# Optimization experiments

Hardware: AMD Instinct MI355X
Metric: run time of the kernel (lower is better)

## Reference

```python
import jax, jax.numpy as jnp
import numpy as np

HEAD = 4
EPS = 1e-12


def _l2norm(x, axis):
    # torch F.normalize: x / max(||x||_2, eps)
    return x / jnp.maximum(jnp.linalg.norm(x, axis=axis, keepdims=True), EPS)


def setup_inputs() -> dict:
    key = jax.random.key(0)
    ks = jax.random.split(key, 12)
    n, t, c, h, w = 2, 7, 96, 96, 96
    inp = {
        "curr_feat": jax.random.normal(ks[0], (n, c, h, w), jnp.float32),
        "index_feat_set_s1": jax.random.normal(ks[1], (n, t, c, h, w), jnp.float32),
        "anchor_feat": jax.random.normal(ks[2], (n, c, h, w), jnp.float32),
        "sparse_feat_set_s1": jax.random.normal(ks[3], (n, t, c, h, w), jnp.float32),
        "sparse_feat_set_s2": jax.random.normal(ks[4], (n, t, c, h, w), jnp.float32),
        "sparse_feat_set_s3": jax.random.normal(ks[5], (n, t, c, h, w), jnp.float32),
        # absolute pixel coordinates (x,y interleaved per frame), mostly in-bounds
        # with a little overshoot to exercise zeros padding of grid_sample
        "location_feat": jax.random.uniform(ks[6], (n, t * 2, h, w), jnp.float32, minval=-2.0, maxval=float(w) + 1.0),
        "proj_w": 0.02 * jax.random.normal(ks[7], (c, c), jnp.float32),
        "proj_b": jnp.zeros((c,), jnp.float32),
        "fusion_w": 0.02 * jax.random.normal(ks[8], (c, 3 * c), jnp.float32),
        "fusion_b": jnp.zeros((c,), jnp.float32),
    }
    return inp


def reference(curr_feat, index_feat_set_s1, anchor_feat, sparse_feat_set_s1,
              sparse_feat_set_s2, sparse_feat_set_s3, location_feat,
              proj_w, proj_b, fusion_w, fusion_b):
    n, c, h, w = anchor_feat.shape
    t = sparse_feat_set_s1.shape[1]
    hd = c // HEAD
    hw = h * w

    # ---- flow-guided nearest grid_sample (align_corners=True, zeros pad) ----
    loc = location_feat.reshape(n, t, 2, h, w)  # (n,t,2,h,w): [x, y] pixel coords
    gx = 2.0 * loc[:, :, 0] / max(w - 1, 1) - 1.0
    gy = 2.0 * loc[:, :, 1] / max(h - 1, 1) - 1.0
    ix = jnp.round((gx + 1.0) * 0.5 * (w - 1))  # nearest (round-half-even, as torch)
    iy = jnp.round((gy + 1.0) * 0.5 * (h - 1))
    valid = (ix >= 0) & (ix <= w - 1) & (iy >= 0) & (iy <= h - 1)
    lin = (jnp.clip(iy, 0, h - 1).astype(jnp.int32) * w
           + jnp.clip(ix, 0, w - 1).astype(jnp.int32)).reshape(n, t, 1, hw)
    vmask = valid.reshape(n, t, 1, hw)

    def sample(f):  # f: (n,t,c,h,w) -> gathered (n,t,c,hw)
        g = jnp.take_along_axis(f.reshape(n, t, c, hw), lin, axis=3)
        return jnp.where(vmask, g, 0.0)

    samp1 = sample(sparse_feat_set_s1)
    samp2 = sample(sparse_feat_set_s2)
    samp3 = sample(sparse_feat_set_s3)
    sampi = sample(index_feat_set_s1)

    # ---- per-pixel multi-head max-correlation over t frames ----
    # queries: normalize over full channel dim c BEFORE splitting into heads
    q = _l2norm(curr_feat.reshape(n, c, hw).transpose(0, 2, 1), -1).reshape(n, hw, HEAD, hd)
    k = _l2norm(sampi.transpose(0, 3, 1, 2), -1).reshape(n, hw, t, HEAD, hd)
    scores = jnp.einsum('npthd,nphd->npht', k, q)  # scale == 1.0 in mode='max'
    corr_soft = jnp.max(scores, axis=3)     # (n,hw,head)
    corr_index = jnp.argmax(scores, axis=3)  # (n,hw,head), first-max like torch

    soft_img = jnp.broadcast_to(corr_soft[..., None], (n, hw, HEAD, hd)) \
                  .reshape(n, h, w, c).transpose(0, 3, 1, 2)  # (n,c,h,w)
    idx = jnp.broadcast_to(corr_index[..., None], (n, hw, HEAD, hd)) \
             .reshape(n, hw, c).transpose(0, 2, 1)[:, None]  # (n,1,c,hw)

    def pick(samp):  # select winning frame per (channel-group, pixel)
        return jnp.take_along_axis(samp, idx, axis=1)[:, 0].reshape(n, c, h, w)

    cat = jnp.concatenate([pick(samp1), pick(samp2), pick(samp3)], axis=1)  # (n,3c,h,w)
    out = jnp.einsum('ndhw,cd->nchw', cat, fusion_w) + fusion_b[None, :, None, None]
    out = out * soft_img
    out = jnp.einsum('nchw,dc->ndhw', out, proj_w) + proj_b[None, :, None, None]
    return out + anchor_feat
```

## Files before the change

### kernel.cpp

```cpp
#include <hip/hip_runtime.h>
#include <hip/hip_bf16.h>

#define N_    2
#define T_    7
#define C_    96
#define H_    96
#define W_    96
#define HW_   9216
#define HEAD_ 4
#define HD_   24
#define C3_   288
#define P_    16
#define QP_   100
#define CATP_ 292
#define NBLK_ (N_ * (HW_ / P_))
#define PLANES_ 14
#define CHUNK_  64
#define NCHUNK_ 144

typedef unsigned int u32;

__device__ __forceinline__ float bits2f(u32 b) {
    union { u32 u; float f; } x; x.u = b; return x.f;
}

__device__ __forceinline__ unsigned short f2bf(float f) {
    union { __hip_bfloat16 h; unsigned short s; } u;
    u.h = __float2bfloat16(f);
    return u.s;
}

template<bool BF16>
__device__ __forceinline__ float ld1(const void* p, int i) {
    if constexpr (BF16) return bits2f(((u32)((const unsigned short*)p)[i]) << 16);
    else                return ((const float*)p)[i];
}

template<bool BF16>
__device__ __forceinline__ void ld4w(const void* p, int i, float w[4]) {
    if constexpr (BF16) {
        const uint2 u = ((const uint2*)p)[i >> 2];
        w[0] = bits2f(u.x << 16);
        w[1] = bits2f(u.x & 0xFFFF0000u);
        w[2] = bits2f(u.y << 16);
        w[3] = bits2f(u.y & 0xFFFF0000u);
    } else {
        const float4 v = *((const float4*)((const float*)p + i));
        w[0] = v.x; w[1] = v.y; w[2] = v.z; w[3] = v.w;
    }
}

template<bool BF16>
__device__ __forceinline__ void st1(void* p, int i, float v) {
    if constexpr (BF16) ((unsigned short*)p)[i] = f2bf(v);
    else                ((float*)p)[i] = v;
}

template<bool BF16>
__device__ __forceinline__ void st4w(void* p, int i, const float v[4]) {
    if constexpr (BF16) {
        uint2 w;
        w.x = (u32)f2bf(v[0]) | ((u32)f2bf(v[1]) << 16);
        w.y = (u32)f2bf(v[2]) | ((u32)f2bf(v[3]) << 16);
        ((uint2*)p)[i >> 2] = w;
    } else {
        *((float4*)((float*)p + i)) = make_float4(v[0], v[1], v[2], v[3]);
    }
}

__device__ __forceinline__ bool block_detect_bf16(const u32* __restrict__ w,
                                                  int tid, int* s_flag) {
    if (tid < 64) {
        u32 x = w[tid];
        u32 f = x & 0x7FFFu;
        int inwin = (f >= 0x3A00u) && (f <= 0x4200u);
        unsigned long long m = __ballot(inwin);
        if (tid == 0) *s_flag = (__popcll(m) >= 40) ? 1 : 0;
    }
    __syncthreads();
    return *s_flag != 0;
}

template<bool BF16>
__device__ __forceinline__ void transp_body(const void* __restrict__ src,
                                            void* __restrict__ dst,
                                            int bx, int tid, char* tileraw) {
    const int pl = bx / NCHUNK_;
    const int x0 = (bx - pl * NCHUNK_) * CHUNK_;
    if constexpr (BF16) {
        unsigned short (*tile)[CHUNK_ + 2] = (unsigned short (*)[CHUNK_ + 2])tileraw;
        const unsigned short* s = (const unsigned short*)src;
        unsigned short* d = (unsigned short*)dst;
        for (int i = tid; i < C_ * (CHUNK_ / 4); i += 256) {
            int ch = i >> 4, xq = i & 15;
            const ushort4 v = *((const ushort4*)(s + (pl * C_ + ch) * HW_ + x0 + 4 * xq));
            tile[ch][4 * xq + 0] = v.x; tile[ch][4 * xq + 1] = v.y;
            tile[ch][4 * xq + 2] = v.z; tile[ch][4 * xq + 3] = v.w;
        }
        __syncthreads();
        for (int i = tid; i < CHUNK_ * (C_ / 4); i += 256) {
            int p = i / 24, cq = i - p * 24;
            ushort4 v;
            v.x = tile[4 * cq + 0][p]; v.y = tile[4 * cq + 1][p];
            v.z = tile[4 * cq + 2][p]; v.w = tile[4 * cq + 3][p];
            *((ushort4*)(d + (pl * HW_ + x0 + p) * C_ + 4 * cq)) = v;
        }
    } else {
        float (*tile)[CHUNK_ + 1] = (float (*)[CHUNK_ + 1])tileraw;
        const float* s = (const float*)src;
        float* d = (float*)dst;
        for (int i = tid; i < C_ * (CHUNK_ / 4); i += 256) {
            int ch = i >> 4, xq = i & 15;
            const float4 v = *((const float4*)(s + (pl * C_ + ch) * HW_ + x0 + 4 * xq));
            tile[ch][4 * xq + 0] = v.x; tile[ch][4 * xq + 1] = v.y;
            tile[ch][4 * xq + 2] = v.z; tile[ch][4 * xq + 3] = v.w;
        }
        __syncthreads();
        for (int i = tid; i < CHUNK_ * (C_ / 4); i += 256) {
            int p = i / 24, cq = i - p * 24;
            float4 v;
            v.x = tile[4 * cq + 0][p]; v.y = tile[4 * cq + 1][p];
            v.z = tile[4 * cq + 2][p]; v.w = tile[4 * cq + 3][p];
            *((float4*)(d + (pl * HW_ + x0 + p) * C_ + 4 * cq)) = v;
        }
    }
}

__global__ __launch_bounds__(256) void transp_kernel(
    const void* __restrict__ a0, const void* __restrict__ a1,
    const void* __restrict__ a2, const void* __restrict__ a3,
    void* __restrict__ dstb, unsigned long long szb,
    const u32* __restrict__ detect_src)
{
    __shared__ __align__(16) char tileraw[C_ * (CHUNK_ + 1) * 4];
    __shared__ int s_flag;
    const int arr = blockIdx.y;
    const void* src = (arr == 0) ? a0 : (arr == 1) ? a1 : (arr == 2) ? a2 : a3;
    void* dst = (char*)dstb + (unsigned long long)arr * szb;
    const int tid = threadIdx.x;
    const bool bf = block_detect_bf16(detect_src, tid, &s_flag);
    if (bf) transp_body<true >(src, dst, blockIdx.x, tid, tileraw);
    else    transp_body<false>(src, dst, blockIdx.x, tid, tileraw);
}

template<bool BF16, bool TGB>
__device__ __forceinline__ void argmax_body(
    const void* __restrict__ curr, const void* __restrict__ loc,
    const void* __restrict__ kT,
    float* __restrict__ ws_best, int* __restrict__ ws_gbase,
    float* s_u, int (*s_lin)[P_], float (*s_red)[8],
    float (*s_best)[HEAD_], int (*s_bidx)[HEAD_], float* s_inv)
{
#define S_Q(pp, ch)  s_u[(pp) * QP_ + (ch)]
#define S_K(pp, ch)  s_u[P_ * QP_ + (pp) * QP_ + (ch)]
    const int tid = threadIdx.x;
    const int b  = blockIdx.x;
    const int nn = b / (HW_ / P_);
    const int p0 = (b - nn * (HW_ / P_)) * P_;

    if (tid < T_ * P_) {
        int t = tid / P_, pp = tid - t * P_;
        int p = p0 + pp;
        float x = ld1<BF16>(loc, (nn * 2 * T_ + 2 * t    ) * HW_ + p);
        float y = ld1<BF16>(loc, (nn * 2 * T_ + 2 * t + 1) * HW_ + p);
        float gx = 2.0f * x / 95.0f - 1.0f;
        float gy = 2.0f * y / 95.0f - 1.0f;
        float fx = (gx + 1.0f) * 0.5f * 95.0f;
        float fy = (gy + 1.0f) * 0.5f * 95.0f;
        float ix = rintf(fx), iy = rintf(fy);
        bool v = (ix >= 0.0f) && (ix <= 95.0f) && (iy >= 0.0f) && (iy <= 95.0f);
        s_lin[t][pp] = v ? ((int)iy * W_ + (int)ix) : -1;
    }
    if (tid >= 128 && tid < 128 + P_ * HEAD_) {
        int q = tid - 128;
        s_best[q >> 2][q & 3] = -3.0e38f; s_bidx[q >> 2][q & 3] = 0;
    }

    for (int i = tid; i < C_ * (P_ / 4); i += 256) {
        int ch = i >> 2, pq = i & 3;
        float w[4];
        ld4w<BF16>(curr, (nn * C_ + ch) * HW_ + p0 + 4 * pq, w);
        S_Q(4 * pq + 0, ch) = w[0]; S_Q(4 * pq + 1, ch) = w[1];
        S_Q(4 * pq + 2, ch) = w[2]; S_Q(4 * pq + 3, ch) = w[3];
    }
    __syncthreads();

    if (tid < P_ * 8) {
        int pp = tid >> 3, j = tid & 7;
        float s = 0.f;
        #pragma unroll
        for (int k = 0; k < 12; ++k) { float v = S_Q(pp, j * 12 + k); s += v * v; }
        s_red[pp][j] = s;
    }
    __syncthreads();
    if (tid < P_) {
        float s = 0.f;
        #pragma unroll
        for (int j = 0; j < 8; ++j) s += s_red[tid][j];
        s_inv[tid] = 1.0f / fmaxf(sqrtf(s), 1e-12f);
    }
    __syncthreads();
    for (int i = tid; i < C_ * P_; i += 256) {
        int pp = i & (P_ - 1), ch = i >> 4;
        S_Q(pp, ch) *= s_inv[pp];
    }

    for (int t = 0; t < T_; ++t) {
        __syncthreads();
        for (int i = tid; i < 24 * P_; i += 256) {
            int pp = i / 24, j = i - pp * 24;
            int lin = s_lin[t][pp];
            float w[4] = {0.f, 0.f, 0.f, 0.f};
            if (lin >= 0) ld4w<BF16>(kT, ((nn * T_ + t) * HW_ + lin) * C_ + 4 * j, w);
            *((float4*)&S_K(pp, 4 * j)) = make_float4(w[0], w[1], w[2], w[3]);
        }
        __syncthreads();
        if (tid < P_ * 8) {
            int pp = tid >> 3, j = tid & 7;
            float s = 0.f;
            #pragma unroll
            for (int k = 0; k < 12; ++k) { float v = S_K(pp, j * 12 + k); s += v * v; }
            s_red[pp][j] = s;
        }
        __syncthreads();
        if (tid < P_) {
            float s = 0.f;
            #pragma unroll
            for (int j = 0; j < 8; ++j) s += s_red[tid][j];
            s_inv[tid] = 1.0f / fmaxf(sqrtf(s), 1e-12f);
        }
        __syncthreads();
        if (tid < P_ * HEAD_) {
            int pp = tid >> 2, h = tid & 3;
            float s = 0.f;
            #pragma unroll
            for (int dq = 0; dq < 6; ++dq) {
                const float4 kv = *((const float4*)&S_K(pp, h * HD_ + 4 * dq));
                const float4 qv = *((const float4*)&S_Q(pp, h * HD_ + 4 * dq));
                s += kv.x * qv.x; s += kv.y * qv.y; s += kv.z * qv.z; s += kv.w * qv.w;
            }
            s *= s_inv[pp];
            if (s > s_best[pp][h]) { s_best[pp][h] = s; s_bidx[pp][h] = t; }
        }
    }
    if (tid < P_ * HEAD_) {
        int pp = tid >> 2, h = tid & 3;
        int bt = s_bidx[pp][h];
        int lin = s_lin[bt][pp];
        int g = (nn * HW_ + p0 + pp) * HEAD_ + h;
        ws_best[g] = s_best[pp][h];
        int gb;
        if (lin < 0)       gb = -1;
        else if (TGB)      gb = ((nn * T_ + bt) * HW_ + lin) * C_;
        else               gb = (nn * T_ + bt) * C_ * HW_ + lin;
        ws_gbase[g] = gb;
    }
#undef S_Q
#undef S_K
}

template<bool TGB>
__global__ __launch_bounds__(256, 8) void argmax_kernel(
    const void* __restrict__ curr, const void* __restrict__ loc,
    const void* __restrict__ kT,
    float* __restrict__ ws_best, int* __restrict__ ws_gbase)
{
    __shared__ __align__(16) float s_u[2 * P_ * QP_];
    __shared__ int   s_lin[T_][P_];
    __shared__ float s_red[P_][8];
    __shared__ float s_best[P_][HEAD_];
    __shared__ int   s_bidx[P_][HEAD_];
    __shared__ float s_inv[P_];
    __shared__ int   s_flag;
    const bool bf = block_detect_bf16((const u32*)curr, threadIdx.x, &s_flag);
    if (bf) argmax_body<true , TGB>(curr, loc, kT, ws_best, ws_gbase, s_u, s_lin, s_red, s_best, s_bidx, s_inv);
    else    argmax_body<false, TGB>(curr, loc, kT, ws_best, ws_gbase, s_u, s_lin, s_red, s_best, s_bidx, s_inv);
}

template<bool BF16, bool TRANS>
__device__ __forceinline__ void catgemv_body(
    const void* __restrict__ anchor, const void* __restrict__ s1,
    const void* __restrict__ s2, const void* __restrict__ s3,
    const void* __restrict__ pw, const void* __restrict__ pb,
    const void* __restrict__ fw, const void* __restrict__ fb,
    void* __restrict__ outp,
    const float* __restrict__ ws_best, const int* __restrict__ ws_gbase,
    float* s_u, float (*s_mid)[QP_], float (*s_best)[HEAD_], int (*s_gbase)[HEAD_])
{
#define S_CAT(pp, d) s_u[(pp) * CATP_ + (d)]
    const int tid = threadIdx.x;
    const int b  = blockIdx.x;
    const int nn = b / (HW_ / P_);
    const int p0 = (b - nn * (HW_ / P_)) * P_;

    if (tid < P_ * HEAD_) {
        int pp = tid >> 2, h = tid & 3;
        int g = (nn * HW_ + p0 + pp) * HEAD_ + h;
        s_best[pp][h]  = ws_best[g];
        s_gbase[pp][h] = ws_gbase[g];
    }
    __syncthreads();

    if constexpr (TRANS) {
        for (int i = tid; i < P_ * 72; i += 256) {
            int px = i / 72, j = i - px * 72;
            int set = j / 24, jj = j - set * 24;
            int gb = s_gbase[px][jj / 6];
            float w[4] = {0.f, 0.f, 0.f, 0.f};
            if (gb >= 0) {
                const void* sp = (set == 0) ? s1 : (set == 1) ? s2 : s3;
                ld4w<BF16>(sp, gb + 4 * jj, w);
            }
            *((float4*)&S_CAT(px, set * C_ + 4 * jj)) = make_float4(w[0], w[1], w[2], w[3]);
        }
    } else {
        for (int i = tid; i < C3_ * P_; i += 256) {
            int pp = i / C3_, d = i - pp * C3_;
            int set = d / C_, ch = d - set * C_;
            int gb = s_gbase[pp][ch / HD_];
            float v = 0.f;
            if (gb >= 0) {
                const void* sp = (set == 0) ? s1 : (set == 1) ? s2 : s3;
                v = ld1<BF16>(sp, gb + ch * HW_);
            }
            S_CAT(pp, d) = v;
        }
    }
    __syncthreads();

    if (tid < 192) {
        const int cp = tid >> 2, pq = tid & 3;
        const int co0 = cp * 2, px0 = pq * 4;
        float acc[2][4];
        #pragma unroll
        for (int r = 0; r < 2; ++r)
            #pragma unroll
            for (int k = 0; k < 4; ++k) acc[r][k] = 0.f;
        for (int d = 0; d < C3_; d += 4) {
            float4 cv[4];
            #pragma unroll
            for (int k = 0; k < 4; ++k) cv[k] = *((const float4*)&S_CAT(px0 + k, d));
            #pragma unroll
            for (int r = 0; r < 2; ++r) {
                float w[4]; ld4w<BF16>(fw, (co0 + r) * C3_ + d, w);
                #pragma unroll
                for (int k = 0; k < 4; ++k)
                    acc[r][k] += w[0] * cv[k].x + w[1] * cv[k].y + w[2] * cv[k].z + w[3] * cv[k].w;
            }
        }
        const int hh = co0 / HD_;
        #pragma unroll
        for (int r = 0; r < 2; ++r) {
            float fbv = ld1<BF16>(fb, co0 + r);
            #pragma unroll
            for (int k = 0; k < 4; ++k)
                s_mid[px0 + k][co0 + r] = (acc[r][k] + fbv) * s_best[px0 + k][hh];
        }
    }
    __syncthreads();

    if (tid < 192) {
        const int dp = tid >> 2, pq = tid & 3;
        const int do0 = dp * 2, px0 = pq * 4;
        float acc[2][4];
        #pragma unroll
        for (int r = 0; r < 2; ++r)
            #pragma unroll
            for (int k = 0; k < 4; ++k) acc[r][k] = 0.f;
        for (int c = 0; c < C_; c += 4) {
            float4 mv[4];
            #pragma unroll
            for (int k = 0; k < 4; ++k) mv[k] = *((const float4*)&s_mid[px0 + k][c]);
            #pragma unroll
            for (int r = 0; r < 2; ++r) {
                float w[4]; ld4w<BF16>(pw, (do0 + r) * C_ + c, w);
                #pragma unroll
                for (int k = 0; k < 4; ++k)
                    acc[r][k] += w[0] * mv[k].x + w[1] * mv[k].y + w[2] * mv[k].z + w[3] * mv[k].w;
            }
        }
        #pragma unroll
        for (int r = 0; r < 2; ++r) {
            float pbv = ld1<BF16>(pb, do0 + r);
            float av[4];
            ld4w<BF16>(anchor, (nn * C_ + do0 + r) * HW_ + p0 + px0, av);
            float res[4];
            #pragma unroll
            for (int k = 0; k < 4; ++k) res[k] = acc[r][k] + pbv + av[k];
            st4w<BF16>(outp, (nn * C_ + do0 + r) * HW_ + p0 + px0, res);
        }
    }
#undef S_CAT
}

template<bool TRANS>
__global__ __launch_bounds__(256, 6) void catgemv_kernel(
    const void* __restrict__ curr, const void* __restrict__ anchor,
    const void* __restrict__ s1, const void* __restrict__ s2,
    const void* __restrict__ s3, const void* __restrict__ pw,
    const void* __restrict__ pb, const void* __restrict__ fw,
    const void* __restrict__ fb, void* __restrict__ outp,
    const float* __restrict__ ws_best, const int* __restrict__ ws_gbase)
{
    __shared__ __align__(16) float s_u[P_ * CATP_];
    __shared__ __align__(16) float s_mid[P_][QP_];
    __shared__ float s_best[P_][HEAD_];
    __shared__ int   s_gbase[P_][HEAD_];
    __shared__ int   s_flag;
    const bool bf = block_detect_bf16((const u32*)curr, threadIdx.x, &s_flag);
    if (bf) catgemv_body<true , TRANS>(anchor, s1, s2, s3, pw, pb, fw, fb, outp, ws_best, ws_gbase,
                                       s_u, s_mid, s_best, s_gbase);
    else    catgemv_body<false, TRANS>(anchor, s1, s2, s3, pw, pb, fw, fb, outp, ws_best, ws_gbase,
                                       s_u, s_mid, s_best, s_gbase);
}

template<bool BF16>
__device__ __forceinline__ void mono_body(
    const void* __restrict__ curr, const void* __restrict__ idxf,
    const void* __restrict__ anchor, const void* __restrict__ s1,
    const void* __restrict__ s2, const void* __restrict__ s3,
    const void* __restrict__ loc, const void* __restrict__ pw,
    const void* __restrict__ pb, const void* __restrict__ fw,
    const void* __restrict__ fb, void* __restrict__ outp,
    float* s_u, float (*s_mid)[QP_], int (*s_lin)[P_], float (*s_red)[8],
    float (*s_best)[HEAD_], int (*s_bidx)[HEAD_], float* s_inv)
{
#define S_Q(pp, ch)  s_u[(pp) * QP_ + (ch)]
#define S_K(pp, ch)  s_u[P_ * QP_ + (pp) * QP_ + (ch)]
#define S_CAT(pp, d) s_u[(pp) * CATP_ + (d)]
    const int tid = threadIdx.x;
    const int b  = blockIdx.x;
    const int nn = b / (HW_ / P_);
    const int p0 = (b - nn * (HW_ / P_)) * P_;

    if (tid < T_ * P_) {
        int t = tid / P_, pp = tid - t * P_;
        int p = p0 + pp;
        float x = ld1<BF16>(loc, (nn * 2 * T_ + 2 * t    ) * HW_ + p);
        float y = ld1<BF16>(loc, (nn * 2 * T_ + 2 * t + 1) * HW_ + p);
        float gx = 2.0f * x / 95.0f - 1.0f;
        float gy = 2.0f * y / 95.0f - 1.0f;
        float fx = (gx + 1.0f) * 0.5f * 95.0f;
        float fy = (gy + 1.0f) * 0.5f * 95.0f;
        float ix = rintf(fx), iy = rintf(fy);
        bool v = (ix >= 0.0f) && (ix <= 95.0f) && (iy >= 0.0f) && (iy <= 95.0f);
        s_lin[t][pp] = v ? ((int)iy * W_ + (int)ix) : -1;
    }
    if (tid >= 128 && tid < 128 + P_ * HEAD_) {
        int q = tid - 128;
        s_best[q >> 2][q & 3] = -3.0e38f; s_bidx[q >> 2][q & 3] = 0;
    }
    for (int i = tid; i < C_ * (P_ / 4); i += 256) {
        int ch = i >> 2, pq = i & 3;
        float w[4];
        ld4w<BF16>(curr, (nn * C_ + ch) * HW_ + p0 + 4 * pq, w);
        S_Q(4 * pq + 0, ch) = w[0]; S_Q(4 * pq + 1, ch) = w[1];
        S_Q(4 * pq + 2, ch) = w[2]; S_Q(4 * pq + 3, ch) = w[3];
    }
    __syncthreads();
    if (tid < P_ * 8) {
        int pp = tid >> 3, j = tid & 7;
        float s = 0.f;
        #pragma unroll
        for (int k = 0; k < 12; ++k) { float v = S_Q(pp, j * 12 + k); s += v * v; }
        s_red[pp][j] = s;
    }
    __syncthreads();
    if (tid < P_) {
        float s = 0.f;
        #pragma unroll
        for (int j = 0; j < 8; ++j) s += s_red[tid][j];
        s_inv[tid] = 1.0f / fmaxf(sqrtf(s), 1e-12f);
    }
    __syncthreads();
    for (int i = tid; i < C_ * P_; i += 256) {
        int pp = i & (P_ - 1), ch = i >> 4;
        S_Q(pp, ch) *= s_inv[pp];
    }
    for (int t = 0; t < T_; ++t) {
        __syncthreads();
        for (int i = tid; i < C_ * P_; i += 256) {
            int ch = i / P_, pp = i - ch * P_;
            int lin = s_lin[t][pp];
            S_K(pp, ch) = (lin >= 0) ? ld1<BF16>(idxf, ((nn * T_ + t) * C_ + ch) * HW_ + lin) : 0.0f;
        }
        __syncthreads();
        if (tid < P_ * 8) {
            int pp = tid >> 3, j = tid & 7;
            float s = 0.f;
            #pragma unroll
            for (int k = 0; k < 12; ++k) { float v = S_K(pp, j * 12 + k); s += v * v; }
            s_red[pp][j] = s;
        }
        __syncthreads();
        if (tid < P_) {
            float s = 0.f;
            #pragma unroll
            for (int j = 0; j < 8; ++j) s += s_red[tid][j];
            s_inv[tid] = 1.0f / fmaxf(sqrtf(s), 1e-12f);
        }
        __syncthreads();
        if (tid < P_ * HEAD_) {
            int pp = tid >> 2, h = tid & 3;
            float s = 0.f;
            #pragma unroll
            for (int dq = 0; dq < 6; ++dq) {
                const float4 kv = *((const float4*)&S_K(pp, h * HD_ + 4 * dq));
                const float4 qv = *((const float4*)&S_Q(pp, h * HD_ + 4 * dq));
                s += kv.x * qv.x; s += kv.y * qv.y; s += kv.z * qv.z; s += kv.w * qv.w;
            }
            s *= s_inv[pp];
            if (s > s_best[pp][h]) { s_best[pp][h] = s; s_bidx[pp][h] = t; }
        }
    }
    __syncthreads();
    for (int i = tid; i < C3_ * P_; i += 256) {
        int pp = i / C3_, d = i - pp * C3_;
        int set = d / C_, ch = d - set * C_;
        int h = ch / HD_;
        int bt = s_bidx[pp][h];
        int lin = s_lin[bt][pp];
        float v = 0.f;
        if (lin >= 0) {
            const void* sp = (set == 0) ? s1 : (set == 1) ? s2 : s3;
            v = ld1<BF16>(sp, ((nn * T_ + bt) * C_ + ch) * HW_ + lin);
        }
        S_CAT(pp, d) = v;
    }
    __syncthreads();
    if (tid < 96) {
        const int cq = tid >> 2, pq = tid & 3;
        const int co0 = cq * 4, px0 = pq * 4;
        float acc[4][4];
        #pragma unroll
        for (int r = 0; r < 4; ++r)
            #pragma unroll
            for (int k = 0; k < 4; ++k) acc[r][k] = 0.f;
        for (int d = 0; d < C3_; d += 4) {
            float4 cv[4];
            #pragma unroll
            for (int k = 0; k < 4; ++k) cv[k] = *((const float4*)&S_CAT(px0 + k, d));
            #pragma unroll
            for (int r = 0; r < 4; ++r) {
                float w[4]; ld4w<BF16>(fw, (co0 + r) * C3_ + d, w);
                #pragma unroll
                for (int k = 0; k < 4; ++k)
                    acc[r][k] += w[0] * cv[k].x + w[1] * cv[k].y + w[2] * cv[k].z + w[3] * cv[k].w;
            }
        }
        const int hh = co0 / HD_;
        #pragma unroll
        for (int r = 0; r < 4; ++r) {
            float fbv = ld1<BF16>(fb, co0 + r);
            #pragma unroll
            for (int k = 0; k < 4; ++k)
                s_mid[px0 + k][co0 + r] = (acc[r][k] + fbv) * s_best[px0 + k][hh];
        }
    }
    __syncthreads();
    if (tid < 96) {
        const int dq = tid >> 2, pq = tid & 3;
        const int do0 = dq * 4, px0 = pq * 4;
        float acc[4][4];
        #pragma unroll
        for (int r = 0; r < 4; ++r)
            #pragma unroll
            for (int k = 0; k < 4; ++k) acc[r][k] = 0.f;
        for (int c = 0; c < C_; c += 4) {
            float4 mv[4];
            #pragma unroll
            for (int k = 0; k < 4; ++k) mv[k] = *((const float4*)&s_mid[px0 + k][c]);
            #pragma unroll
            for (int r = 0; r < 4; ++r) {
                float w[4]; ld4w<BF16>(pw, (do0 + r) * C_ + c, w);
                #pragma unroll
                for (int k = 0; k < 4; ++k)
                    acc[r][k] += w[0] * mv[k].x + w[1] * mv[k].y + w[2] * mv[k].z + w[3] * mv[k].w;
            }
        }
        #pragma unroll
        for (int r = 0; r < 4; ++r) {
            float pbv = ld1<BF16>(pb, do0 + r);
            float av[4];
            ld4w<BF16>(anchor, (nn * C_ + do0 + r) * HW_ + p0 + px0, av);
            float res[4];
            #pragma unroll
            for (int k = 0; k < 4; ++k) res[k] = acc[r][k] + pbv + av[k];
            st4w<BF16>(outp, (nn * C_ + do0 + r) * HW_ + p0 + px0, res);
        }
    }
#undef S_Q
#undef S_K
#undef S_CAT
}

__global__ __launch_bounds__(256) void mono_kernel(
    const void* __restrict__ curr, const void* __restrict__ idxf,
    const void* __restrict__ anchor, const void* __restrict__ s1,
    const void* __restrict__ s2, const void* __restrict__ s3,
    const void* __restrict__ loc, const void* __restrict__ pw,
    const void* __restrict__ pb, const void* __restrict__ fw,
    const void* __restrict__ fb, void* __restrict__ outp)
{
    __shared__ __align__(16) float s_u[P_ * CATP_];
    __shared__ __align__(16) float s_mid[P_][QP_];
    __shared__ int   s_lin[T_][P_];
    __shared__ float s_red[P_][8];
    __shared__ float s_best[P_][HEAD_];
    __shared__ int   s_bidx[P_][HEAD_];
    __shared__ float s_inv[P_];
    __shared__ int   s_flag;
    const bool bf = block_detect_bf16((const u32*)curr, threadIdx.x, &s_flag);
    if (bf) mono_body<true >(curr, idxf, anchor, s1, s2, s3, loc, pw, pb, fw, fb, outp,
                             s_u, s_mid, s_lin, s_red, s_best, s_bidx, s_inv);
    else    mono_body<false>(curr, idxf, anchor, s1, s2, s3, loc, pw, pb, fw, fb, outp,
                             s_u, s_mid, s_lin, s_red, s_best, s_bidx, s_inv);
}

extern "C" void kernel_launch(void* const* d_in, const int* in_sizes, int n_in,
                              void* d_out, int out_size, void* d_ws, size_t ws_size,
                              hipStream_t stream) {
    (void)in_sizes; (void)n_in; (void)out_size;
    const unsigned long long SZB  = (unsigned long long)N_ * T_ * HW_ * C_ * 4ull;
    const unsigned long long AUXB = (unsigned long long)N_ * HW_ * HEAD_ * 4ull;
    char* wsb = (char*)d_ws;

    dim3 grid(NBLK_), block(256);
    if (ws_size >= 4 * SZB + 2 * AUXB) {
        void*  kT       = wsb;
        void*  s1T      = wsb + SZB;
        void*  s2T      = wsb + 2 * SZB;
        void*  s3T      = wsb + 3 * SZB;
        float* ws_best  = (float*)(wsb + 4 * SZB);
        int*   ws_gbase = (int*)  (wsb + 4 * SZB + AUXB);
        transp_kernel<<<dim3(PLANES_ * NCHUNK_, 4), 256, 0, stream>>>(
            d_in[1], d_in[3], d_in[4], d_in[5], wsb, SZB, (const u32*)d_in[0]);
        argmax_kernel<true><<<grid, block, 0, stream>>>(d_in[0], d_in[6], kT, ws_best, ws_gbase);
        catgemv_kernel<true><<<grid, block, 0, stream>>>(d_in[0], d_in[2], s1T, s2T, s3T,
                                                         d_in[7], d_in[8], d_in[9], d_in[10],
                                                         d_out, ws_best, ws_gbase);
    } else if (ws_size >= SZB + 2 * AUXB) {
        void*  kT       = wsb;
        float* ws_best  = (float*)(wsb + SZB);
        int*   ws_gbase = (int*)  (wsb + SZB + AUXB);
        transp_kernel<<<dim3(PLANES_ * NCHUNK_, 1), 256, 0, stream>>>(
            d_in[1], d_in[1], d_in[1], d_in[1], wsb, SZB, (const u32*)d_in[0]);
        argmax_kernel<false><<<grid, block, 0, stream>>>(d_in[0], d_in[6], kT, ws_best, ws_gbase);
        catgemv_kernel<false><<<grid, block, 0, stream>>>(d_in[0], d_in[2], d_in[3], d_in[4], d_in[5],
                                                          d_in[7], d_in[8], d_in[9], d_in[10],
                                                          d_out, ws_best, ws_gbase);
    } else {
        mono_kernel<<<grid, block, 0, stream>>>(d_in[0], d_in[1], d_in[2], d_in[3], d_in[4],
                                                d_in[5], d_in[6], d_in[7], d_in[8], d_in[9],
                                                d_in[10], d_out);
    }
}
```

Baseline: 312.0 us.

## Overlap argmax with s1-s3 transposes in one fused launch; swizzle transpose tile

The transpose of the index set now runs alone first. The argmax blocks and the transposes of the three sparse sets are then merged into a single fused kernel, so the compute-bound argmax can overlap the bandwidth-bound transposes. The shared-memory transpose tile is changed to an XOR-swizzled, pixel-major layout so the write-back reads whole 4-wide vectors instead of four scalar reads. The fused kernel uses launch bounds of 6 blocks per SM and a larger shared buffer, which may lower occupancy for the argmax part.

```diff
diff --git a/kernel.cpp b/kernel.cpp
--- a/kernel.cpp
+++ b/kernel.cpp
@@ -17,6 +17,7 @@
 #define PLANES_ 14
 #define CHUNK_  64
 #define NCHUNK_ 144
+#define TBLK_ (PLANES_ * NCHUNK_)
 
 typedef unsigned int u32;
 
@@ -82,45 +83,49 @@
 }
 
 template<bool BF16>
-__device__ __forceinline__ void transp_body(const void* __restrict__ src,
-                                            void* __restrict__ dst,
-                                            int bx, int tid, char* tileraw) {
-    const int pl = bx / NCHUNK_;
-    const int x0 = (bx - pl * NCHUNK_) * CHUNK_;
+__device__ __forceinline__ void transp_swz(const void* __restrict__ src,
+                                           void* __restrict__ dst,
+                                           int pl, int x0, int tid, char* raw) {
     if constexpr (BF16) {
-        unsigned short (*tile)[CHUNK_ + 2] = (unsigned short (*)[CHUNK_ + 2])tileraw;
+        unsigned short* tile = (unsigned short*)raw;
         const unsigned short* s = (const unsigned short*)src;
         unsigned short* d = (unsigned short*)dst;
         for (int i = tid; i < C_ * (CHUNK_ / 4); i += 256) {
             int ch = i >> 4, xq = i & 15;
             const ushort4 v = *((const ushort4*)(s + (pl * C_ + ch) * HW_ + x0 + 4 * xq));
-            tile[ch][4 * xq + 0] = v.x; tile[ch][4 * xq + 1] = v.y;
-            tile[ch][4 * xq + 2] = v.z; tile[ch][4 * xq + 3] = v.w;
+            int g = (ch >> 2) ^ (xq & 7);
+            int chl = ch & 3;
+            tile[(4 * xq + 0) * 96 + 4 * g + chl] = v.x;
+            tile[(4 * xq + 1) * 96 + 4 * g + chl] = v.y;
+            tile[(4 * xq + 2) * 96 + 4 * g + chl] = v.z;
+            tile[(4 * xq + 3) * 96 + 4 * g + chl] = v.w;
         }
         __syncthreads();
         for (int i = tid; i < CHUNK_ * (C_ / 4); i += 256) {
             int p = i / 24, cq = i - p * 24;
-            ushort4 v;
-            v.x = tile[4 * cq + 0][p]; v.y = tile[4 * cq + 1][p];
-            v.z = tile[4 * cq + 2][p]; v.w = tile[4 * cq + 3][p];
+            int g = cq ^ ((p >> 2) & 7);
+            const ushort4 v = *((const ushort4*)&tile[p * 96 + 4 * g]);
             *((ushort4*)(d + (pl * HW_ + x0 + p) * C_ + 4 * cq)) = v;
         }
     } else {
-        float (*tile)[CHUNK_ + 1] = (float (*)[CHUNK_ + 1])tileraw;
+        float* tile = (float*)raw;
         const float* s = (const float*)src;
         float* d = (float*)dst;
         for (int i = tid; i < C_ * (CHUNK_ / 4); i += 256) {
             int ch = i >> 4, xq = i & 15;
             const float4 v = *((const float4*)(s + (pl * C_ + ch) * HW_ + x0 + 4 * xq));
-            tile[ch][4 * xq + 0] = v.x; tile[ch][4 * xq + 1] = v.y;
-            tile[ch][4 * xq + 2] = v.z; tile[ch][4 * xq + 3] = v.w;
+            int g = (ch >> 2) ^ (xq & 7);
+            int chl = ch & 3;
+            tile[(4 * xq + 0) * 96 + 4 * g + chl] = v.x;
+            tile[(4 * xq + 1) * 96 + 4 * g + chl] = v.y;
+            tile[(4 * xq + 2) * 96 + 4 * g + chl] = v.z;
+            tile[(4 * xq + 3) * 96 + 4 * g + chl] = v.w;
         }
         __syncthreads();
         for (int i = tid; i < CHUNK_ * (C_ / 4); i += 256) {
             int p = i / 24, cq = i - p * 24;
-            float4 v;
-            v.x = tile[4 * cq + 0][p]; v.y = tile[4 * cq + 1][p];
-            v.z = tile[4 * cq + 2][p]; v.w = tile[4 * cq + 3][p];
+            int g = cq ^ ((p >> 2) & 7);
+            const float4 v = *((const float4*)&tile[p * 96 + 4 * g]);
             *((float4*)(d + (pl * HW_ + x0 + p) * C_ + 4 * cq)) = v;
         }
     }
@@ -132,15 +137,17 @@
     void* __restrict__ dstb, unsigned long long szb,
     const u32* __restrict__ detect_src)
 {
-    __shared__ __align__(16) char tileraw[C_ * (CHUNK_ + 1) * 4];
+    __shared__ __align__(16) char raw[24832];
     __shared__ int s_flag;
     const int arr = blockIdx.y;
     const void* src = (arr == 0) ? a0 : (arr == 1) ? a1 : (arr == 2) ? a2 : a3;
     void* dst = (char*)dstb + (unsigned long long)arr * szb;
     const int tid = threadIdx.x;
+    const int pl = blockIdx.x / NCHUNK_;
+    const int x0 = (blockIdx.x - pl * NCHUNK_) * CHUNK_;
     const bool bf = block_detect_bf16(detect_src, tid, &s_flag);
-    if (bf) transp_body<true >(src, dst, blockIdx.x, tid, tileraw);
-    else    transp_body<false>(src, dst, blockIdx.x, tid, tileraw);
+    if (bf) transp_swz<true >(src, dst, pl, x0, tid, raw);
+    else    transp_swz<false>(src, dst, pl, x0, tid, raw);
 }
 
 template<bool BF16, bool TGB>
@@ -275,6 +282,43 @@
     const bool bf = block_detect_bf16((const u32*)curr, threadIdx.x, &s_flag);
     if (bf) argmax_body<true , TGB>(curr, loc, kT, ws_best, ws_gbase, s_u, s_lin, s_red, s_best, s_bidx, s_inv);
     else    argmax_body<false, TGB>(curr, loc, kT, ws_best, ws_gbase, s_u, s_lin, s_red, s_best, s_bidx, s_inv);
+}
+
+__global__ __launch_bounds__(256, 6) void fused_kernel(
+    const void* __restrict__ curr, const void* __restrict__ loc,
+    const void* __restrict__ kT,
+    const void* __restrict__ s1, const void* __restrict__ s2,
+    const void* __restrict__ s3,
+    void* __restrict__ s123T, unsigned long long szb,
+    float* __restrict__ ws_best, int* __restrict__ ws_gbase)
+{
+    __shared__ __align__(16) char raw[24832];
+    __shared__ int s_flag;
+    const int tid = threadIdx.x;
+    const bool bf = block_detect_bf16((const u32*)curr, tid, &s_flag);
+    const int bx = blockIdx.x;
+    if (bx < NBLK_) {
+        float* s_u            = (float*)raw;
+        int   (*s_lin)[P_]    = (int(*)[P_])   (raw + 12800);
+        float (*s_red)[8]     = (float(*)[8])  (raw + 13248);
+        float (*s_best)[HEAD_]= (float(*)[HEAD_])(raw + 13760);
+        int   (*s_bidx)[HEAD_]= (int(*)[HEAD_]) (raw + 14016);
+        float* s_inv          = (float*)(raw + 14272);
+        if (bf) argmax_body<true , true>(curr, loc, kT, ws_best, ws_gbase,
+                                         s_u, s_lin, s_red, s_best, s_bidx, s_inv);
+        else    argmax_body<false, true>(curr, loc, kT, ws_best, ws_gbase,
+                                         s_u, s_lin, s_red, s_best, s_bidx, s_inv);
+    } else {
+        int t = bx - NBLK_;
+        int arr = t / TBLK_;
+        int bxx = t - arr * TBLK_;
+        const void* src = (arr == 0) ? s1 : (arr == 1) ? s2 : s3;
+        void* dst = (char*)s123T + (unsigned long long)arr * szb;
+        int pl = bxx / NCHUNK_;
+        int x0 = (bxx - pl * NCHUNK_) * CHUNK_;
+        if (bf) transp_swz<true >(src, dst, pl, x0, tid, raw);
+        else    transp_swz<false>(src, dst, pl, x0, tid, raw);
+    }
 }
 
 template<bool BF16, bool TRANS>
@@ -628,23 +672,23 @@
     dim3 grid(NBLK_), block(256);
     if (ws_size >= 4 * SZB + 2 * AUXB) {
         void*  kT       = wsb;
-        void*  s1T      = wsb + SZB;
-        void*  s2T      = wsb + 2 * SZB;
-        void*  s3T      = wsb + 3 * SZB;
+        void*  s123T    = wsb + SZB;
         float* ws_best  = (float*)(wsb + 4 * SZB);
         int*   ws_gbase = (int*)  (wsb + 4 * SZB + AUXB);
-        transp_kernel<<<dim3(PLANES_ * NCHUNK_, 4), 256, 0, stream>>>(
-            d_in[1], d_in[3], d_in[4], d_in[5], wsb, SZB, (const u32*)d_in[0]);
-        argmax_kernel<true><<<grid, block, 0, stream>>>(d_in[0], d_in[6], kT, ws_best, ws_gbase);
-        catgemv_kernel<true><<<grid, block, 0, stream>>>(d_in[0], d_in[2], s1T, s2T, s3T,
-                                                         d_in[7], d_in[8], d_in[9], d_in[10],
-                                                         d_out, ws_best, ws_gbase);
+        transp_kernel<<<dim3(TBLK_, 1), 256, 0, stream>>>(
+            d_in[1], d_in[1], d_in[1], d_in[1], kT, SZB, (const u32*)d_in[0]);
+        fused_kernel<<<dim3(NBLK_ + 3 * TBLK_), 256, 0, stream>>>(
+            d_in[0], d_in[6], kT, d_in[3], d_in[4], d_in[5], s123T, SZB, ws_best, ws_gbase);
+        catgemv_kernel<true><<<grid, block, 0, stream>>>(
+            d_in[0], d_in[2],
+            (char*)s123T, (char*)s123T + SZB, (char*)s123T + 2 * SZB,
+            d_in[7], d_in[8], d_in[9], d_in[10], d_out, ws_best, ws_gbase);
     } else if (ws_size >= SZB + 2 * AUXB) {
         void*  kT       = wsb;
         float* ws_best  = (float*)(wsb + SZB);
         int*   ws_gbase = (int*)  (wsb + SZB + AUXB);
-        transp_kernel<<<dim3(PLANES_ * NCHUNK_, 1), 256, 0, stream>>>(
-            d_in[1], d_in[1], d_in[1], d_in[1], wsb, SZB, (const u32*)d_in[0]);
+        transp_kernel<<<dim3(TBLK_, 1), 256, 0, stream>>>(
+            d_in[1], d_in[1], d_in[1], d_in[1], kT, SZB, (const u32*)d_in[0]);
         argmax_kernel<false><<<grid, block, 0, stream>>>(d_in[0], d_in[6], kT, ws_best, ws_gbase);
         catgemv_kernel<false><<<grid, block, 0, stream>>>(d_in[0], d_in[2], d_in[3], d_in[4], d_in[5],
                                                           d_in[7], d_in[8], d_in[9], d_in[10],
```

Result: faster. 302.5 us (-3.0%).
